# Kernel optimization log

Measured on AMD Instinct MI355X. Metric: run time of the kernel, lower is better.

The kernel has to match this reference:

```python
import jax, jax.numpy as jnp
import numpy as np

N_IDX = 4
N_LATENT = 6
D_IDX = 2 ** N_IDX
D_LATENT = 2 ** N_LATENT
D = D_IDX * D_LATENT  # 1024
TIME_EMBED = 128
BATCH = 32


def _build_H():
    # S_plus |k> = |(k+1) mod d_idx>, H_idx = S_plus + S_plus^T, H = H_idx kron I_latent
    S_plus = np.zeros((D_IDX, D_IDX), dtype=np.float32)
    for k in range(D_IDX):
        S_plus[(k + 1) % D_IDX, k] = 1.0
    H_idx = S_plus + S_plus.T
    H = np.kron(H_idx, np.eye(D_LATENT, dtype=np.float32))
    return jnp.asarray(H)


def setup_inputs() -> dict:
    key = jax.random.key(0)
    k_rho, k_t, k_w1, k_b1, k_w2, k_b2 = jax.random.split(key, 6)
    # PSD density-like rho so the trace normalization is well-conditioned
    A = jax.random.normal(k_rho, (BATCH, D, D), dtype=jnp.float32)
    rho = jnp.einsum('bij,bkj->bik', A, A) / D
    t = jax.random.uniform(k_t, (BATCH,), dtype=jnp.float32)
    # lambda_net: Linear(1, E) -> SiLU -> Linear(E, 1) -> Tanh (torch Linear: weight (out,in))
    w1 = jax.random.normal(k_w1, (TIME_EMBED, 1), dtype=jnp.float32) * 1.0
    b1 = jax.random.uniform(k_b1, (TIME_EMBED,), dtype=jnp.float32, minval=-1.0, maxval=1.0)
    w2 = jax.random.normal(k_w2, (1, TIME_EMBED), dtype=jnp.float32) * (1.0 / np.sqrt(TIME_EMBED))
    b2 = jax.random.uniform(k_b2, (1,), dtype=jnp.float32, minval=-0.09, maxval=0.09)
    H = _build_H()
    return {'rho': rho, 't': t, 'w1': w1, 'b1': b1, 'w2': w2, 'b2': b2, 'H': H}


def reference(rho, t, w1, b1, w2, b2, H):
    # lambda(t) = 0.1 * tanh(Linear(SiLU(Linear(t))))
    x = t[:, None]  # (B, 1)
    h = jax.nn.silu(x @ w1.T + b1)  # (B, E)
    lam = jnp.tanh(h @ w2.T + b2)[:, 0] * 0.1  # (B,)
    # Shared eigendecomposition of constant symmetric H
    eigvals, eigvecs = jnp.linalg.eigh(H)  # (D,), (D, D)
    exp_diag = jnp.exp(-lam[:, None] * eigvals[None, :])  # (B, D)
    # U_b = V diag(exp_diag_b) V^T, batched
    U = jnp.einsum('id,bd,jd->bij', eigvecs, exp_diag, eigvecs)  # (B, D, D)
    rho_out = jnp.einsum('bij,bjk,blk->bil', U, rho, U)  # U rho U^T
    trace = jnp.trace(rho_out, axis1=-2, axis2=-1)[:, None, None]
    return rho_out / jnp.maximum(trace, 1e-8)
```

## Files before the change

kernel.cpp:

```cpp
#include <hip/hip_runtime.h>
#include <stdint.h>

#define DI 16
#define DD 1024
#define NB 32
#define PI8  0.39269908169872414f

#define AS1 __attribute__((address_space(1)))
#define AS3 __attribute__((address_space(3)))

#define WS_E   0
#define WS_TRP (NB*256)

__global__ __launch_bounds__(256)
void k_trace(const float* __restrict__ rho,
             const float* __restrict__ t,
             const float* __restrict__ w1,
             const float* __restrict__ b1,
             const float* __restrict__ w2,
             const float* __restrict__ b2,
             float* __restrict__ ws) {
    int x = blockIdx.x;
    int b = blockIdx.y;
    int tid = threadIdx.x;
    __shared__ float lam_sh;
    __shared__ float ck[16];
    __shared__ float gam[16];
    __shared__ float part[4];

    if (tid < 64) {
        float tb = t[b];
        float z0 = tb * w1[tid]      + b1[tid];
        float z1 = tb * w1[tid + 64] + b1[tid + 64];
        float h0 = z0 / (1.0f + expf(-z0));
        float h1 = z1 / (1.0f + expf(-z1));
        float v = h0 * w2[tid] + h1 * w2[tid + 64];
        #pragma unroll
        for (int off = 32; off; off >>= 1) v += __shfl_down(v, off, 64);
        if (tid == 0) lam_sh = tanhf(v + b2[0]) * 0.1f;
    }
    if (tid >= 64 && tid < 80) ck[tid - 64] = cosf(PI8 * (float)(tid - 64));
    __syncthreads();
    float lam = lam_sh;

    if (x == 0) {
        int i = tid >> 4, j = tid & 15, r = (i - j) & 15;
        float se = 0.0f;
        #pragma unroll
        for (int k = 0; k < 16; k++)
            se += expf(-2.0f * lam * ck[k]) * ck[(k * r) & 15];
        ws[WS_E + b * 256 + tid] = se * 0.0625f;
    }

    if (tid < 16) {
        float sg = 0.0f;
        #pragma unroll
        for (int k = 0; k < 16; k++)
            sg += expf(-4.0f * lam * ck[k]) * ck[(k * tid) & 15];
        gam[tid] = sg * 0.0625f;
    }
    __syncthreads();

    const float* bbase = rho + (size_t)b * DD * DD;
    int nA = 16 - x;
    float s = 0.0f;
    #pragma unroll
    for (int it = 0; it < 5; it++) {
        int idx = it * 256 + tid;
        if (idx < 17 * 64) {
            int pr = idx >> 6, p = idx & 63;
            int c  = (pr < nA) ? x : 15 - x;
            int d  = (pr < nA) ? x + pr : (15 - x) + (pr - nA);
            int r  = d - c;
            float w = gam[r] * (r ? 2.0f : 1.0f);
            s += w * bbase[(size_t)(c * 64 + p) * DD + d * 64 + p];
        }
    }
    #pragma unroll
    for (int off = 32; off; off >>= 1) s += __shfl_down(s, off, 64);
    if ((tid & 63) == 0) part[tid >> 6] = s;
    __syncthreads();
    if (tid == 0)
        ws[WS_TRP + b * 8 + x] = part[0] + part[1] + part[2] + part[3];
}

__global__ __launch_bounds__(256, 2)
void k_main(const float* __restrict__ rho,
            const float* __restrict__ ws,
            float* __restrict__ out) {
    __shared__ __align__(16) float S[16 * 512];
    __shared__ float Es[256];
    __shared__ float sinv_sh;

    int qt  = blockIdx.x;
    int p   = blockIdx.y;
    int b   = blockIdx.z;
    int tid = threadIdx.x;
    int q0  = qt * 32;

    if (tid < 64) {
        ((float4*)Es)[tid] = ((const float4*)(ws + WS_E + b * 256))[tid];
        float v = (tid < 8) ? ws[WS_TRP + b * 8 + tid] : 0.0f;
        #pragma unroll
        for (int off = 32; off; off >>= 1) v += __shfl_down(v, off, 64);
        if (tid == 0) sinv_sh = 1.0f / fmaxf(v, 1e-8f);
    }

    const float* rbase = rho + (size_t)b * (DD * DD) + q0;
    #pragma unroll
    for (int it = 0; it < 8; it++) {
        int g  = it * 256 + tid;
        int c  = g >> 7;
        int r  = g & 127;
        int d  = r >> 3;
        int q4 = r & 7;
        const float* ga = rbase + (size_t)(c * 64 + p) * DD + d * 64 + q4 * 4;
        int gw = it * 256 + (tid & ~63);
        unsigned fo = (unsigned)((gw >> 7) * 512 + (gw & 127) * 4);
        __builtin_amdgcn_global_load_lds((const AS1 uint32_t*)ga,
                                         (AS3 uint32_t*)&S[fo], 16, 0, 0);
    }

    asm volatile("s_waitcnt vmcnt(4) lgkmcnt(0)\n\ts_barrier" ::: "memory");
    __builtin_amdgcn_sched_barrier(0);

    int ah = tid >> 7;
    int d  = (tid >> 3) & 15;
    int qq = (tid & 7) * 4;
    {
        float4 acc[8];
        #pragma unroll
        for (int i = 0; i < 8; i++) acc[i] = make_float4(0.f, 0.f, 0.f, 0.f);

        #pragma unroll
        for (int c = 0; c < 8; c++) {
            float4 s4 = *(float4*)&S[c * 512 + d * 32 + qq];
            float4 e0 = *(float4*)&Es[c * 16 + ah * 8];
            float4 e1 = *(float4*)&Es[c * 16 + ah * 8 + 4];
            acc[0].x += e0.x * s4.x; acc[0].y += e0.x * s4.y; acc[0].z += e0.x * s4.z; acc[0].w += e0.x * s4.w;
            acc[1].x += e0.y * s4.x; acc[1].y += e0.y * s4.y; acc[1].z += e0.y * s4.z; acc[1].w += e0.y * s4.w;
            acc[2].x += e0.z * s4.x; acc[2].y += e0.z * s4.y; acc[2].z += e0.z * s4.z; acc[2].w += e0.z * s4.w;
            acc[3].x += e0.w * s4.x; acc[3].y += e0.w * s4.y; acc[3].z += e0.w * s4.z; acc[3].w += e0.w * s4.w;
            acc[4].x += e1.x * s4.x; acc[4].y += e1.x * s4.y; acc[4].z += e1.x * s4.z; acc[4].w += e1.x * s4.w;
            acc[5].x += e1.y * s4.x; acc[5].y += e1.y * s4.y; acc[5].z += e1.y * s4.z; acc[5].w += e1.y * s4.w;
            acc[6].x += e1.z * s4.x; acc[6].y += e1.z * s4.y; acc[6].z += e1.z * s4.z; acc[6].w += e1.z * s4.w;
            acc[7].x += e1.w * s4.x; acc[7].y += e1.w * s4.y; acc[7].z += e1.w * s4.z; acc[7].w += e1.w * s4.w;
        }

        asm volatile("s_waitcnt vmcnt(0)\n\ts_barrier" ::: "memory");
        __builtin_amdgcn_sched_barrier(0);

        #pragma unroll
        for (int c = 8; c < 16; c++) {
            float4 s4 = *(float4*)&S[c * 512 + d * 32 + qq];
            float4 e0 = *(float4*)&Es[c * 16 + ah * 8];
            float4 e1 = *(float4*)&Es[c * 16 + ah * 8 + 4];
            acc[0].x += e0.x * s4.x; acc[0].y += e0.x * s4.y; acc[0].z += e0.x * s4.z; acc[0].w += e0.x * s4.w;
            acc[1].x += e0.y * s4.x; acc[1].y += e0.y * s4.y; acc[1].z += e0.y * s4.z; acc[1].w += e0.y * s4.w;
            acc[2].x += e0.z * s4.x; acc[2].y += e0.z * s4.y; acc[2].z += e0.z * s4.z; acc[2].w += e0.z * s4.w;
            acc[3].x += e0.w * s4.x; acc[3].y += e0.w * s4.y; acc[3].z += e0.w * s4.z; acc[3].w += e0.w * s4.w;
            acc[4].x += e1.x * s4.x; acc[4].y += e1.x * s4.y; acc[4].z += e1.x * s4.z; acc[4].w += e1.x * s4.w;
            acc[5].x += e1.y * s4.x; acc[5].y += e1.y * s4.y; acc[5].z += e1.y * s4.z; acc[5].w += e1.y * s4.w;
            acc[6].x += e1.z * s4.x; acc[6].y += e1.z * s4.y; acc[6].z += e1.z * s4.z; acc[6].w += e1.z * s4.w;
            acc[7].x += e1.w * s4.x; acc[7].y += e1.w * s4.y; acc[7].z += e1.w * s4.z; acc[7].w += e1.w * s4.w;
        }

        __syncthreads();
        #pragma unroll
        for (int ai = 0; ai < 8; ai++)
            *(float4*)&S[(ah * 8 + ai) * 512 + d * 32 + qq] = acc[ai];
    }
    __syncthreads();

    {
        int bp = (tid >> 3) & 15;
        float Eb[16];
        #pragma unroll
        for (int j4 = 0; j4 < 4; j4++) {
            float4 e = *(float4*)&Es[bp * 16 + j4 * 4];
            Eb[4 * j4 + 0] = e.x; Eb[4 * j4 + 1] = e.y; Eb[4 * j4 + 2] = e.z; Eb[4 * j4 + 3] = e.w;
        }
        float sinv = sinv_sh;
        float* obase = out + (size_t)b * (DD * DD) + (size_t)p * DD + bp * 64 + q0 + qq;
        #pragma unroll
        for (int ai = 0; ai < 8; ai++) {
            int a = ah * 8 + ai;
            float4 acc = make_float4(0.f, 0.f, 0.f, 0.f);
            #pragma unroll
            for (int dd = 0; dd < 16; dd++) {
                float4 t4 = *(float4*)&S[a * 512 + dd * 32 + qq];
                acc.x += Eb[dd] * t4.x; acc.y += Eb[dd] * t4.y;
                acc.z += Eb[dd] * t4.z; acc.w += Eb[dd] * t4.w;
            }
            acc.x *= sinv; acc.y *= sinv; acc.z *= sinv; acc.w *= sinv;
            *(float4*)(obase + (size_t)a * (64 * DD)) = acc;
        }
    }
}

extern "C" void kernel_launch(void* const* d_in, const int* in_sizes, int n_in,
                              void* d_out, int out_size, void* d_ws, size_t ws_size,
                              hipStream_t stream) {
    const float* rho = (const float*)d_in[0];
    const float* t   = (const float*)d_in[1];
    const float* w1  = (const float*)d_in[2];
    const float* b1  = (const float*)d_in[3];
    const float* w2  = (const float*)d_in[4];
    const float* b2  = (const float*)d_in[5];
    float* out = (float*)d_out;
    float* ws  = (float*)d_ws;

    k_trace<<<dim3(8, NB), 256, 0, stream>>>(rho, t, w1, b1, w2, b2, ws);
    k_main <<<dim3(2, 64, NB), 256, 0, stream>>>(rho, ws, out);
}
```

Measured before the change: 64.26 us.

## Merge q-tile blocks into one block that prefetches both halves into separate LDS buffers

Each block now handles both 32-column q halves for a given (p,b) instead of launching two blocks. Both halves are issued as async global-to-LDS loads up front, so the second half's load overlaps the first half's compute and stores. This halves the grid and doubles shared memory per block (about 65KB), which may reduce occupancy below the declared two blocks per CU. The vmcnt waits are hand-tuned to the load counts, and the step-2 global stores also count against vmcnt, which the final vmcnt(0) wait handles conservatively.

```diff
diff --git a/kernel.cpp b/kernel.cpp
--- a/kernel.cpp
+++ b/kernel.cpp
@@ -84,19 +84,60 @@
         ws[WS_TRP + b * 8 + x] = part[0] + part[1] + part[2] + part[3];
 }
 
+__device__ __forceinline__ void fma8(const float* Sb, const float* Es,
+                                     int c, int d, int qq, int ah, float4* acc) {
+    float4 s4 = *(const float4*)&Sb[c * 512 + d * 32 + qq];
+    float4 e0 = *(const float4*)&Es[c * 16 + ah * 8];
+    float4 e1 = *(const float4*)&Es[c * 16 + ah * 8 + 4];
+    acc[0].x += e0.x * s4.x; acc[0].y += e0.x * s4.y; acc[0].z += e0.x * s4.z; acc[0].w += e0.x * s4.w;
+    acc[1].x += e0.y * s4.x; acc[1].y += e0.y * s4.y; acc[1].z += e0.y * s4.z; acc[1].w += e0.y * s4.w;
+    acc[2].x += e0.z * s4.x; acc[2].y += e0.z * s4.y; acc[2].z += e0.z * s4.z; acc[2].w += e0.z * s4.w;
+    acc[3].x += e0.w * s4.x; acc[3].y += e0.w * s4.y; acc[3].z += e0.w * s4.z; acc[3].w += e0.w * s4.w;
+    acc[4].x += e1.x * s4.x; acc[4].y += e1.x * s4.y; acc[4].z += e1.x * s4.z; acc[4].w += e1.x * s4.w;
+    acc[5].x += e1.y * s4.x; acc[5].y += e1.y * s4.y; acc[5].z += e1.y * s4.z; acc[5].w += e1.y * s4.w;
+    acc[6].x += e1.z * s4.x; acc[6].y += e1.z * s4.y; acc[6].z += e1.z * s4.z; acc[6].w += e1.z * s4.w;
+    acc[7].x += e1.w * s4.x; acc[7].y += e1.w * s4.y; acc[7].z += e1.w * s4.z; acc[7].w += e1.w * s4.w;
+}
+
+__device__ __forceinline__ void step2_store(const float* Sb, const float* Es,
+                                            float sinv, float* out,
+                                            int b, int p, int qbase,
+                                            int ah, int qq, int tid) {
+    int bp = (tid >> 3) & 15;
+    float Eb[16];
+    #pragma unroll
+    for (int j4 = 0; j4 < 4; j4++) {
+        float4 e = *(const float4*)&Es[bp * 16 + j4 * 4];
+        Eb[4 * j4 + 0] = e.x; Eb[4 * j4 + 1] = e.y; Eb[4 * j4 + 2] = e.z; Eb[4 * j4 + 3] = e.w;
+    }
+    float* obase = out + (size_t)b * (DD * DD) + (size_t)p * DD + bp * 64 + qbase + qq;
+    #pragma unroll
+    for (int ai = 0; ai < 8; ai++) {
+        int a = ah * 8 + ai;
+        float4 acc = make_float4(0.f, 0.f, 0.f, 0.f);
+        #pragma unroll
+        for (int dd = 0; dd < 16; dd++) {
+            float4 t4 = *(const float4*)&Sb[a * 512 + dd * 32 + qq];
+            acc.x += Eb[dd] * t4.x; acc.y += Eb[dd] * t4.y;
+            acc.z += Eb[dd] * t4.z; acc.w += Eb[dd] * t4.w;
+        }
+        acc.x *= sinv; acc.y *= sinv; acc.z *= sinv; acc.w *= sinv;
+        *(float4*)(obase + (size_t)a * (64 * DD)) = acc;
+    }
+}
+
 __global__ __launch_bounds__(256, 2)
 void k_main(const float* __restrict__ rho,
             const float* __restrict__ ws,
             float* __restrict__ out) {
-    __shared__ __align__(16) float S[16 * 512];
+    __shared__ __align__(16) float S1[16 * 512];
+    __shared__ __align__(16) float S2[16 * 512];
     __shared__ float Es[256];
     __shared__ float sinv_sh;
 
-    int qt  = blockIdx.x;
-    int p   = blockIdx.y;
-    int b   = blockIdx.z;
+    int p   = blockIdx.x;
+    int b   = blockIdx.y;
     int tid = threadIdx.x;
-    int q0  = qt * 32;
 
     if (tid < 64) {
         ((float4*)Es)[tid] = ((const float4*)(ws + WS_E + b * 256))[tid];
@@ -106,7 +147,7 @@
         if (tid == 0) sinv_sh = 1.0f / fmaxf(v, 1e-8f);
     }
 
-    const float* rbase = rho + (size_t)b * (DD * DD) + q0;
+    const float* rbase = rho + (size_t)b * (DD * DD);
     #pragma unroll
     for (int it = 0; it < 8; it++) {
         int g  = it * 256 + tid;
@@ -118,84 +159,70 @@
         int gw = it * 256 + (tid & ~63);
         unsigned fo = (unsigned)((gw >> 7) * 512 + (gw & 127) * 4);
         __builtin_amdgcn_global_load_lds((const AS1 uint32_t*)ga,
-                                         (AS3 uint32_t*)&S[fo], 16, 0, 0);
-    }
-
-    asm volatile("s_waitcnt vmcnt(4) lgkmcnt(0)\n\ts_barrier" ::: "memory");
-    __builtin_amdgcn_sched_barrier(0);
+                                         (AS3 uint32_t*)&S1[fo], 16, 0, 0);
+    }
+    #pragma unroll
+    for (int it = 0; it < 8; it++) {
+        int g  = it * 256 + tid;
+        int c  = g >> 7;
+        int r  = g & 127;
+        int d  = r >> 3;
+        int q4 = r & 7;
+        const float* ga = rbase + (size_t)(c * 64 + p) * DD + 32 + d * 64 + q4 * 4;
+        int gw = it * 256 + (tid & ~63);
+        unsigned fo = (unsigned)((gw >> 7) * 512 + (gw & 127) * 4);
+        __builtin_amdgcn_global_load_lds((const AS1 uint32_t*)ga,
+                                         (AS3 uint32_t*)&S2[fo], 16, 0, 0);
+    }
 
     int ah = tid >> 7;
     int d  = (tid >> 3) & 15;
     int qq = (tid & 7) * 4;
+
+    asm volatile("s_waitcnt vmcnt(12) lgkmcnt(0)\n\ts_barrier" ::: "memory");
+    __builtin_amdgcn_sched_barrier(0);
+
     {
         float4 acc[8];
         #pragma unroll
         for (int i = 0; i < 8; i++) acc[i] = make_float4(0.f, 0.f, 0.f, 0.f);
-
-        #pragma unroll
-        for (int c = 0; c < 8; c++) {
-            float4 s4 = *(float4*)&S[c * 512 + d * 32 + qq];
-            float4 e0 = *(float4*)&Es[c * 16 + ah * 8];
-            float4 e1 = *(float4*)&Es[c * 16 + ah * 8 + 4];
-            acc[0].x += e0.x * s4.x; acc[0].y += e0.x * s4.y; acc[0].z += e0.x * s4.z; acc[0].w += e0.x * s4.w;
-            acc[1].x += e0.y * s4.x; acc[1].y += e0.y * s4.y; acc[1].z += e0.y * s4.z; acc[1].w += e0.y * s4.w;
-            acc[2].x += e0.z * s4.x; acc[2].y += e0.z * s4.y; acc[2].z += e0.z * s4.z; acc[2].w += e0.z * s4.w;
-            acc[3].x += e0.w * s4.x; acc[3].y += e0.w * s4.y; acc[3].z += e0.w * s4.z; acc[3].w += e0.w * s4.w;
-            acc[4].x += e1.x * s4.x; acc[4].y += e1.x * s4.y; acc[4].z += e1.x * s4.z; acc[4].w += e1.x * s4.w;
-            acc[5].x += e1.y * s4.x; acc[5].y += e1.y * s4.y; acc[5].z += e1.y * s4.z; acc[5].w += e1.y * s4.w;
-            acc[6].x += e1.z * s4.x; acc[6].y += e1.z * s4.y; acc[6].z += e1.z * s4.z; acc[6].w += e1.z * s4.w;
-            acc[7].x += e1.w * s4.x; acc[7].y += e1.w * s4.y; acc[7].z += e1.w * s4.z; acc[7].w += e1.w * s4.w;
-        }
-
-        asm volatile("s_waitcnt vmcnt(0)\n\ts_barrier" ::: "memory");
+        #pragma unroll
+        for (int c = 0; c < 8; c++) fma8(S1, Es, c, d, qq, ah, acc);
+
+        asm volatile("s_waitcnt vmcnt(8)\n\ts_barrier" ::: "memory");
         __builtin_amdgcn_sched_barrier(0);
 
         #pragma unroll
-        for (int c = 8; c < 16; c++) {
-            float4 s4 = *(float4*)&S[c * 512 + d * 32 + qq];
-            float4 e0 = *(float4*)&Es[c * 16 + ah * 8];
-            float4 e1 = *(float4*)&Es[c * 16 + ah * 8 + 4];
-            acc[0].x += e0.x * s4.x; acc[0].y += e0.x * s4.y; acc[0].z += e0.x * s4.z; acc[0].w += e0.x * s4.w;
-            acc[1].x += e0.y * s4.x; acc[1].y += e0.y * s4.y; acc[1].z += e0.y * s4.z; acc[1].w += e0.y * s4.w;
-            acc[2].x += e0.z * s4.x; acc[2].y += e0.z * s4.y; acc[2].z += e0.z * s4.z; acc[2].w += e0.z * s4.w;
-            acc[3].x += e0.w * s4.x; acc[3].y += e0.w * s4.y; acc[3].z += e0.w * s4.z; acc[3].w += e0.w * s4.w;
-            acc[4].x += e1.x * s4.x; acc[4].y += e1.x * s4.y; acc[4].z += e1.x * s4.z; acc[4].w += e1.x * s4.w;
-            acc[5].x += e1.y * s4.x; acc[5].y += e1.y * s4.y; acc[5].z += e1.y * s4.z; acc[5].w += e1.y * s4.w;
-            acc[6].x += e1.z * s4.x; acc[6].y += e1.z * s4.y; acc[6].z += e1.z * s4.z; acc[6].w += e1.z * s4.w;
-            acc[7].x += e1.w * s4.x; acc[7].y += e1.w * s4.y; acc[7].z += e1.w * s4.z; acc[7].w += e1.w * s4.w;
-        }
-
-        __syncthreads();
+        for (int c = 8; c < 16; c++) fma8(S1, Es, c, d, qq, ah, acc);
+
+        asm volatile("s_waitcnt lgkmcnt(0)\n\ts_barrier" ::: "memory");
         #pragma unroll
         for (int ai = 0; ai < 8; ai++)
-            *(float4*)&S[(ah * 8 + ai) * 512 + d * 32 + qq] = acc[ai];
-    }
-    __syncthreads();
+            *(float4*)&S1[(ah * 8 + ai) * 512 + d * 32 + qq] = acc[ai];
+    }
+    asm volatile("s_waitcnt lgkmcnt(0)\n\ts_barrier" ::: "memory");
+
+    float sinv = sinv_sh;
+    step2_store(S1, Es, sinv, out, b, p, 0, ah, qq, tid);
+
+    asm volatile("s_waitcnt vmcnt(0)\n\ts_barrier" ::: "memory");
+    __builtin_amdgcn_sched_barrier(0);
 
     {
-        int bp = (tid >> 3) & 15;
-        float Eb[16];
-        #pragma unroll
-        for (int j4 = 0; j4 < 4; j4++) {
-            float4 e = *(float4*)&Es[bp * 16 + j4 * 4];
-            Eb[4 * j4 + 0] = e.x; Eb[4 * j4 + 1] = e.y; Eb[4 * j4 + 2] = e.z; Eb[4 * j4 + 3] = e.w;
-        }
-        float sinv = sinv_sh;
-        float* obase = out + (size_t)b * (DD * DD) + (size_t)p * DD + bp * 64 + q0 + qq;
-        #pragma unroll
-        for (int ai = 0; ai < 8; ai++) {
-            int a = ah * 8 + ai;
-            float4 acc = make_float4(0.f, 0.f, 0.f, 0.f);
-            #pragma unroll
-            for (int dd = 0; dd < 16; dd++) {
-                float4 t4 = *(float4*)&S[a * 512 + dd * 32 + qq];
-                acc.x += Eb[dd] * t4.x; acc.y += Eb[dd] * t4.y;
-                acc.z += Eb[dd] * t4.z; acc.w += Eb[dd] * t4.w;
-            }
-            acc.x *= sinv; acc.y *= sinv; acc.z *= sinv; acc.w *= sinv;
-            *(float4*)(obase + (size_t)a * (64 * DD)) = acc;
-        }
-    }
+        float4 acc[8];
+        #pragma unroll
+        for (int i = 0; i < 8; i++) acc[i] = make_float4(0.f, 0.f, 0.f, 0.f);
+        #pragma unroll
+        for (int c = 0; c < 16; c++) fma8(S2, Es, c, d, qq, ah, acc);
+
+        asm volatile("s_waitcnt lgkmcnt(0)\n\ts_barrier" ::: "memory");
+        #pragma unroll
+        for (int ai = 0; ai < 8; ai++)
+            *(float4*)&S2[(ah * 8 + ai) * 512 + d * 32 + qq] = acc[ai];
+    }
+    asm volatile("s_waitcnt lgkmcnt(0)\n\ts_barrier" ::: "memory");
+
+    step2_store(S2, Es, sinv, out, b, p, 32, ah, qq, tid);
 }
 
 extern "C" void kernel_launch(void* const* d_in, const int* in_sizes, int n_in,
@@ -211,5 +238,5 @@
     float* ws  = (float*)d_ws;
 
     k_trace<<<dim3(8, NB), 256, 0, stream>>>(rho, t, w1, b1, w2, b2, ws);
-    k_main <<<dim3(2, 64, NB), 256, 0, stream>>>(rho, ws, out);
-}
+    k_main <<<dim3(64, NB), 256, 0, stream>>>(rho, ws, out);
+}
```

Measured after the change: 69.49 us. 8.1% more time.
